# Performance work log

Measured on AMD Instinct MI355X. Metric: run time of the kernel, lower is better.

## Reference

```python
import jax, jax.numpy as jnp
import numpy as np

D_MODEL = 1024
N_HEADS = 16
N_GROUPS = 4
D_HEAD = D_MODEL // N_HEADS  # 64
HPG = N_HEADS // N_GROUPS    # heads per KV group = 4
B, T = 2, 2048


def _rope(x):
    # x: [B, H, T, D]; interleaved even/odd rotary, matching the torch module
    t, d = x.shape[2], x.shape[3]
    pos = jnp.arange(t, dtype=jnp.float32)[:, None]                      # [T,1]
    freq = jnp.exp(-(jnp.arange(0, d, 2, dtype=jnp.float32) / d)
                   * jnp.log(jnp.float32(10000.0)))                      # [D/2]
    angle = pos * freq                                                   # [T, D/2]
    cos, sin = jnp.cos(angle), jnp.sin(angle)
    xe, xo = x[..., ::2], x[..., 1::2]
    re = xe * cos - xo * sin
    ro = xe * sin + xo * cos
    return jnp.stack([re, ro], axis=-1).reshape(x.shape)


def setup_inputs() -> dict:
    key = jax.random.key(0)
    ks = jax.random.split(key, 10)
    s = 0.02
    return {
        "x":  jax.random.normal(ks[0], (B, T, D_MODEL), dtype=jnp.float32),
        "Wq": jax.random.normal(ks[1], (D_MODEL, D_MODEL), dtype=jnp.float32) * s,
        "bq": jax.random.normal(ks[2], (D_MODEL,), dtype=jnp.float32) * s,
        "Wk": jax.random.normal(ks[3], (D_MODEL, N_GROUPS * D_HEAD), dtype=jnp.float32) * s,
        "bk": jax.random.normal(ks[4], (N_GROUPS * D_HEAD,), dtype=jnp.float32) * s,
        "Wv": jax.random.normal(ks[5], (D_MODEL, N_GROUPS * D_HEAD), dtype=jnp.float32) * s,
        "bv": jax.random.normal(ks[6], (N_GROUPS * D_HEAD,), dtype=jnp.float32) * s,
        "Wo": jax.random.normal(ks[7], (D_MODEL, D_MODEL), dtype=jnp.float32) * s,
        "bo": jax.random.normal(ks[8], (D_MODEL,), dtype=jnp.float32) * s,
    }


def reference(x, Wq, bq, Wk, bk, Wv, bv, Wo, bo):
    b, t, _ = x.shape
    q = (x @ Wq + bq).reshape(b, t, N_HEADS, D_HEAD).transpose(0, 2, 1, 3)    # [B,H,T,D]
    k = (x @ Wk + bk).reshape(b, t, N_GROUPS, D_HEAD).transpose(0, 2, 1, 3)   # [B,G,T,D]
    v = (x @ Wv + bv).reshape(b, t, N_GROUPS, D_HEAD).transpose(0, 2, 1, 3)
    # GQA broadcast: idx = arange(n_heads) // heads_per_group  ==  repeat each group HPG times
    k = jnp.repeat(k, HPG, axis=1)                                            # [B,H,T,D]
    v = jnp.repeat(v, HPG, axis=1)
    q = _rope(q)
    k = _rope(k)
    scale = jnp.float32(np.sqrt(D_HEAD))
    scores = jnp.einsum('bhtd,bhsd->bhts', q, k) / scale                      # [B,H,T,T]
    causal = jnp.tril(jnp.ones((t, t), dtype=bool))
    scores = jnp.where(causal, scores, -jnp.inf)
    probs = jax.nn.softmax(scores, axis=-1)
    # dropout(p=0.05) is identity in eval mode
    attn = jnp.einsum('bhts,bhsd->bhtd', probs, v)
    out = attn.transpose(0, 2, 1, 3).reshape(b, t, N_HEADS * D_HEAD)
    return out @ Wo + bo
```

## Files before the change

kernel.cpp:

```cpp
#include <hip/hip_runtime.h>
#include <stdint.h>

typedef unsigned short u16;
typedef __attribute__((ext_vector_type(4))) float f32x4;
typedef __attribute__((ext_vector_type(8))) short bf16x8;
typedef __attribute__((ext_vector_type(4))) short bf16x4;

#define T_SEQ 2048
#define DM 1024
#define NH 16
#define NG 4
#define DH 64
#define QSCALE 0.18033688011112042f

__device__ __forceinline__ u16 f2bf(float f) {
    union { float f; uint32_t u; } v; v.f = f;
    uint32_t r = (v.u + 0x7FFFu + ((v.u >> 16) & 1u)) >> 16;
    return (u16)r;
}
__device__ __forceinline__ float bf2f(u16 u) {
    union { uint32_t u; float f; } v; v.u = ((uint32_t)u) << 16;
    return v.f;
}
__device__ __forceinline__ float fexp2(float x) {
#if __has_builtin(__builtin_amdgcn_exp2f)
    return __builtin_amdgcn_exp2f(x);
#else
    return exp2f(x);
#endif
}
__device__ __forceinline__ uint32_t cvtpk_bf16(float a, float b) {
    uint32_t r;
    asm("v_cvt_pk_bf16_f32 %0, %1, %2" : "=v"(r) : "v"(a), "v"(b));
    return r;
}

#if __has_builtin(__builtin_amdgcn_mfma_f32_16x16x16_bf16)
__device__ __forceinline__ f32x4 mfma16(bf16x4 a, bf16x4 b, f32x4 c) {
    return __builtin_amdgcn_mfma_f32_16x16x16_bf16(a, b, c, 0, 0, 0);
}
#elif __has_builtin(__builtin_amdgcn_mfma_f32_16x16x16bf16_1k)
__device__ __forceinline__ f32x4 mfma16(bf16x4 a, bf16x4 b, f32x4 c) {
    return __builtin_amdgcn_mfma_f32_16x16x16bf16_1k(a, b, c, 0, 0, 0);
}
#else
__device__ __forceinline__ f32x4 mfma16(bf16x4 a, bf16x4 b, f32x4 c) {
    asm("v_mfma_f32_16x16x16_bf16 %0, %1, %2, %0" : "+v"(c) : "v"(a), "v"(b));
    return c;
}
#endif

__device__ __forceinline__ void async16(const void* g, void* l) {
    __builtin_amdgcn_global_load_lds(
        (const __attribute__((address_space(1))) void*)g,
        (__attribute__((address_space(3))) void*)l,
        16, 0, 0);
}

__global__ __launch_bounds__(256) void k_prep(
    const float* __restrict__ x, u16* __restrict__ xb,
    const float* __restrict__ Wq, const float* __restrict__ Wk,
    const float* __restrict__ Wv, const float* __restrict__ Wo,
    u16* __restrict__ wqkvt, u16* __restrict__ wot,
    const float* __restrict__ bq, const float* __restrict__ bk,
    const float* __restrict__ bv, float* __restrict__ bqkv,
    float2* __restrict__ tbl) {
    int blk = blockIdx.x;
    int tid = threadIdx.x;
    if (blk < 2048) {
        int i = blk * 256 + tid;
        const float4* p = (const float4*)x + (size_t)i * 2;
        float4 a = p[0], b = p[1];
        bf16x8 v;
        v[0] = (short)f2bf(a.x); v[1] = (short)f2bf(a.y);
        v[2] = (short)f2bf(a.z); v[3] = (short)f2bf(a.w);
        v[4] = (short)f2bf(b.x); v[5] = (short)f2bf(b.y);
        v[6] = (short)f2bf(b.z); v[7] = (short)f2bf(b.w);
        ((bf16x8*)xb)[i] = v;
        return;
    }
    int t = blk - 2048;
    if (t >= 2560) {
        int u = t - 2560;
        if (u < 6) {
            int i = u * 256 + tid;
            if (i < 1536) {
                float v;
                if (i < 1024) v = bq[i];
                else if (i < 1280) v = bk[i - 1024];
                else v = bv[i - 1280];
                bqkv[i] = v;
            }
        } else {
            int idx = (u - 6) * 256 + tid;
            int tt = idx >> 5, i = idx & 31;
            float freq = exp2f(-(float)i * (13.287712379549449f / 32.0f));
            float ang = (float)tt * freq;
            tbl[idx] = make_float2(cosf(ang), sinf(ang));
        }
        return;
    }
    const float* src; u16* dst; int N;
    if (t < 1024)      { src = Wq; dst = wqkvt;                      N = 1024; }
    else if (t < 1280) { t -= 1024; src = Wk; dst = wqkvt + (size_t)1024 * 1024; N = 256; }
    else if (t < 1536) { t -= 1280; src = Wv; dst = wqkvt + (size_t)1280 * 1024; N = 256; }
    else               { t -= 1536; src = Wo; dst = wot;             N = 1024; }
    int ntiles = N >> 5;
    int n0 = (t % ntiles) * 32, k0 = (t / ntiles) * 32;
    __shared__ float tile[32][33];
    int tx = tid & 31, ty = tid >> 5;
#pragma unroll
    for (int q = 0; q < 4; q++)
        tile[ty + q * 8][tx] = src[(size_t)(k0 + ty + q * 8) * N + n0 + tx];
    __syncthreads();
#pragma unroll
    for (int q = 0; q < 4; q++)
        dst[(size_t)(n0 + ty + q * 8) * 1024 + k0 + tx] = f2bf(tile[tx][ty + q * 8]);
}

__global__ __launch_bounds__(256) void k_gemm_qkv(
    const u16* __restrict__ A, const u16* __restrict__ Bt,
    const float* __restrict__ bias, const float2* __restrict__ tbl,
    u16* __restrict__ Qo, u16* __restrict__ Ko, u16* __restrict__ Vto) {
    const int K = 1024;
    __shared__ __align__(16) u16 As[64 * 64];
    __shared__ __align__(16) u16 Bs[128 * 64];
    int tid = threadIdx.x;
    int lane = tid & 63, wid = tid >> 6;
    int wr = wid >> 1, wc = wid & 1;
    int l15 = lane & 15, lhi = lane >> 4;
    int row0 = blockIdx.y * 64, col0 = blockIdx.x * 128;
    f32x4 acc[2][4] = {};

    for (int k0 = 0; k0 < K; k0 += 64) {
#pragma unroll
        for (int i = 0; i < 2; i++) {
            int c = i * 256 + tid;
            int r = c >> 3, ch = c & 7;
            int sch = ch ^ (r & 7);
            async16(A + (size_t)(row0 + r) * K + k0 + sch * 8, &As[c * 8]);
        }
#pragma unroll
        for (int i = 0; i < 4; i++) {
            int c = i * 256 + tid;
            int r = c >> 3, ch = c & 7;
            int sch = ch ^ (r & 7);
            async16(Bt + (size_t)(col0 + r) * K + k0 + sch * 8, &Bs[c * 8]);
        }
        __syncthreads();
#pragma unroll
        for (int ks = 0; ks < 2; ks++) {
            bf16x8 af[2], bfr[4];
#pragma unroll
            for (int m = 0; m < 2; m++) {
                int r = wr * 32 + m * 16 + l15;
                int kb = (ks * 64 + lhi * 16) ^ ((r & 7) << 4);
                af[m] = *(const bf16x8*)((const char*)As + r * 128 + kb);
            }
#pragma unroll
            for (int n = 0; n < 4; n++) {
                int r = wc * 64 + n * 16 + l15;
                int kb = (ks * 64 + lhi * 16) ^ ((r & 7) << 4);
                bfr[n] = *(const bf16x8*)((const char*)Bs + r * 128 + kb);
            }
#pragma unroll
            for (int m = 0; m < 2; m++)
#pragma unroll
                for (int n = 0; n < 4; n++)
                    acc[m][n] = __builtin_amdgcn_mfma_f32_16x16x32_bf16(
                        af[m], bfr[n], acc[m][n], 0, 0, 0);
        }
        __syncthreads();
    }

    int type = (col0 >= 1280) ? 2 : (col0 >= 1024 ? 1 : 0);
    int rbase = row0 + wr * 32;
#pragma unroll
    for (int n = 0; n < 4; n++) {
        int col = col0 + wc * 64 + n * 16 + l15;
        float bv = bias[col];
        if (type == 2) {
            int cc = col - 1280;
            int g = cc >> 6, d = cc & 63;
#pragma unroll
            for (int m = 0; m < 2; m++)
#pragma unroll
                for (int i = 0; i < 4; i++) {
                    int rowg = rbase + m * 16 + lhi * 4 + i;
                    int t = rowg & (T_SEQ - 1), b = rowg >> 11;
                    int sp = t ^ ((d & 1) << 2);
                    Vto[(((size_t)(b * NG + g)) * DH + d) * T_SEQ + sp] =
                        f2bf(acc[m][n][i] + bv);
                }
        } else {
            float ssgn = (col & 1) ? 1.f : -1.f;
            int ip = (col & 63) >> 1;
#pragma unroll
            for (int m = 0; m < 2; m++)
#pragma unroll
                for (int i = 0; i < 4; i++) {
                    int rowg = rbase + m * 16 + lhi * 4 + i;
                    int t = rowg & (T_SEQ - 1), b = rowg >> 11;
                    float v = acc[m][n][i] + bv;
                    float other = __shfl_xor(v, 1);
                    float2 cs = tbl[t * 32 + ip];
                    float out = v * cs.x + other * cs.y * ssgn;
                    if (type == 0) {
                        int h = col >> 6, d = col & 63;
                        Qo[(((size_t)(b * NH + h)) * T_SEQ + t) * DH + d] =
                            f2bf(out * QSCALE);
                    } else {
                        int cc = col - 1024;
                        int g = cc >> 6, d = cc & 63;
                        Ko[(((size_t)(b * NG + g)) * T_SEQ + t) * DH + d] = f2bf(out);
                    }
                }
        }
    }
}

__global__ __launch_bounds__(256) void k_gemm_out(
    const u16* __restrict__ A, const u16* __restrict__ Bt,
    const float* __restrict__ bias, float* __restrict__ C,
    int M, int N, int K) {
    __shared__ __align__(16) u16 As[64 * 64];
    __shared__ __align__(16) u16 Bs[128 * 64];
    int tid = threadIdx.x;
    int lane = tid & 63, wid = tid >> 6;
    int wr = wid >> 1, wc = wid & 1;
    int l15 = lane & 15, lhi = lane >> 4;
    int row0 = blockIdx.y * 64, col0 = blockIdx.x * 128;
    f32x4 acc[2][4] = {};

    for (int k0 = 0; k0 < K; k0 += 64) {
#pragma unroll
        for (int i = 0; i < 2; i++) {
            int c = i * 256 + tid;
            int r = c >> 3, ch = c & 7;
            int sch = ch ^ (r & 7);
            async16(A + (size_t)(row0 + r) * K + k0 + sch * 8, &As[c * 8]);
        }
#pragma unroll
        for (int i = 0; i < 4; i++) {
            int c = i * 256 + tid;
            int r = c >> 3, ch = c & 7;
            int sch = ch ^ (r & 7);
            async16(Bt + (size_t)(col0 + r) * K + k0 + sch * 8, &Bs[c * 8]);
        }
        __syncthreads();
#pragma unroll
        for (int ks = 0; ks < 2; ks++) {
            bf16x8 af[2], bfr[4];
#pragma unroll
            for (int m = 0; m < 2; m++) {
                int r = wr * 32 + m * 16 + l15;
                int kb = (ks * 64 + lhi * 16) ^ ((r & 7) << 4);
                af[m] = *(const bf16x8*)((const char*)As + r * 128 + kb);
            }
#pragma unroll
            for (int n = 0; n < 4; n++) {
                int r = wc * 64 + n * 16 + l15;
                int kb = (ks * 64 + lhi * 16) ^ ((r & 7) << 4);
                bfr[n] = *(const bf16x8*)((const char*)Bs + r * 128 + kb);
            }
#pragma unroll
            for (int m = 0; m < 2; m++)
#pragma unroll
                for (int n = 0; n < 4; n++)
                    acc[m][n] = __builtin_amdgcn_mfma_f32_16x16x32_bf16(
                        af[m], bfr[n], acc[m][n], 0, 0, 0);
        }
        __syncthreads();
    }
#pragma unroll
    for (int n = 0; n < 4; n++) {
        int col = col0 + wc * 64 + n * 16 + l15;
        float bv = bias[col];
#pragma unroll
        for (int m = 0; m < 2; m++) {
            int row = row0 + wr * 32 + m * 16 + lhi * 4;
#pragma unroll
            for (int i = 0; i < 4; i++)
                C[(size_t)(row + i) * N + col] = acc[m][n][i] + bv;
        }
    }
}

__global__ __launch_bounds__(256) void k_attn(
    const u16* __restrict__ Q, const u16* __restrict__ K,
    const u16* __restrict__ Vt, u16* __restrict__ Aout) {
    int i0 = blockIdx.x;
    int u = i0 >> 5;
    int qt = (u < 16) ? (31 - u) : (u - 16);
    int bh = i0 & 31;
    int b = bh >> 4, h = bh & 15, g = h >> 2;
    int tid = threadIdx.x;
    int lane = tid & 63, wid = tid >> 6;
    int l15 = lane & 15, lhi = lane >> 4;

    const u16* Kp = K + ((size_t)(b * NG + g)) * T_SEQ * DH;
    const u16* Vp = Vt + ((size_t)(b * NG + g)) * DH * T_SEQ;

    __shared__ __align__(16) u16 Ks[2][64 * 64];
    __shared__ __align__(16) u16 Vs[2][64 * 64];

    const u16* Qp = Q + ((size_t)bh * T_SEQ + qt * 64) * DH;
    bf16x8 qf[2];
#pragma unroll
    for (int ks = 0; ks < 2; ks++)
        qf[ks] = *(const bf16x8*)(Qp + (size_t)(wid * 16 + l15) * DH + ks * 32 + lhi * 8);

    f32x4 of[4] = {};
    float m_i = -3.0e38f, l_i = 0.f;

    int nt = qt + 1;
    int swz = (l15 & 7) << 4;

    int c0 = tid, c1 = tid + 256;
    int rk0 = c0 >> 3, rk1 = c1 >> 3;
    int sk0 = (c0 & 7) ^ (rk0 & 7);
    int sk1 = (c1 & 7) ^ (rk1 & 7);
    int sv0 = (c0 & 7) ^ ((rk0 >> 1) & 7);
    int sv1 = (c1 & 7) ^ ((rk1 >> 1) & 7);
    const u16* kg0 = Kp + rk0 * DH + sk0 * 8;
    const u16* kg1 = Kp + rk1 * DH + sk1 * 8;
    const u16* vg0 = Vp + (size_t)rk0 * T_SEQ + sv0 * 8;
    const u16* vg1 = Vp + (size_t)rk1 * T_SEQ + sv1 * 8;

    async16(kg0, &Ks[0][c0 * 8]);
    async16(kg1, &Ks[0][c1 * 8]);
    async16(vg0, &Vs[0][c0 * 8]);
    async16(vg1, &Vs[0][c1 * 8]);
    __syncthreads();

#pragma unroll 1
    for (int it = 0; it < nt; it++) {
        int cur = it & 1;
        if (it + 1 < nt) {
            int nx = cur ^ 1;
            int ko = (it + 1) << 12;
            int vo = (it + 1) << 6;
            async16(kg0 + ko, &Ks[nx][c0 * 8]);
            async16(kg1 + ko, &Ks[nx][c1 * 8]);
            async16(vg0 + vo, &Vs[nx][c0 * 8]);
            async16(vg1 + vo, &Vs[nx][c1 * 8]);
        }
        const u16* Kc = Ks[cur];
        const u16* Vc = Vs[cur];

        f32x4 sf[4] = {};
        __builtin_amdgcn_s_setprio(1);
#pragma unroll
        for (int ks = 0; ks < 2; ks++)
#pragma unroll
            for (int n = 0; n < 4; n++) {
                int kb = (ks * 64 + lhi * 16) ^ swz;
                bf16x8 kf = *(const bf16x8*)((const char*)Kc + (n * 16 + l15) * 128 + kb);
                sf[n] = __builtin_amdgcn_mfma_f32_16x16x32_bf16(kf, qf[ks], sf[n], 0, 0, 0);
            }
        __builtin_amdgcn_s_setprio(0);

        if (it == nt - 1) {
            int qrow = qt * 64 + wid * 16 + l15;
            int sb = it * 64 + lhi * 4;
#pragma unroll
            for (int n = 0; n < 4; n++)
#pragma unroll
                for (int i = 0; i < 4; i++)
                    if (sb + n * 16 + i > qrow) sf[n][i] = -3.0e38f;
        }

        float pmt = sf[0][0];
#pragma unroll
        for (int n = 0; n < 4; n++)
#pragma unroll
            for (int i = 0; i < 4; i++)
                pmt = fmaxf(pmt, sf[n][i]);
        if (!__all(pmt - m_i <= 8.f)) {
#pragma unroll
            for (int off = 16; off <= 32; off <<= 1)
                pmt = fmaxf(pmt, __shfl_xor(pmt, off));
            float mn = fmaxf(m_i, pmt);
            float sc = fexp2(m_i - mn);
            m_i = mn;
            l_i *= sc;
            float sc4[4];
#pragma unroll
            for (int i = 0; i < 4; i++)
                sc4[i] = __shfl(sc, lhi * 4 + i);
#pragma unroll
            for (int n = 0; n < 4; n++)
#pragma unroll
                for (int i = 0; i < 4; i++)
                    of[n][i] *= sc4[i];
        }
        bf16x4 pa[4];
#pragma unroll
        for (int n = 0; n < 4; n++) {
#pragma unroll
            for (int i = 0; i < 4; i++) {
                float p = fexp2(sf[n][i] - m_i);
                sf[n][i] = p;
                l_i += p;
            }
            union { uint32_t u[2]; bf16x4 v; } pu;
            pu.u[0] = cvtpk_bf16(sf[n][0], sf[n][1]);
            pu.u[1] = cvtpk_bf16(sf[n][2], sf[n][3]);
            pa[n] = pu.v;
        }

        __builtin_amdgcn_s_setprio(1);
#pragma unroll
        for (int nd = 0; nd < 4; nd++) {
            int rowb = (nd * 16 + l15) * 128;
#pragma unroll
            for (int n = 0; n < 4; n++) {
                int kb = ((4 * n + lhi) ^ l15) << 3;
                bf16x4 vf = *(const bf16x4*)((const char*)Vc + rowb + kb);
                of[nd] = mfma16(pa[n], vf, of[nd]);
            }
        }
        __builtin_amdgcn_s_setprio(0);
        __syncthreads();
    }

#pragma unroll
    for (int off = 16; off <= 32; off <<= 1)
        l_i += __shfl_xor(l_i, off);
    float lq[4];
#pragma unroll
    for (int i = 0; i < 4; i++)
        lq[i] = __shfl(l_i, lhi * 4 + i);
#pragma unroll
    for (int n = 0; n < 4; n++)
#pragma unroll
        for (int i = 0; i < 4; i++) {
            int trow = qt * 64 + wid * 16 + lhi * 4 + i;
            float v = of[n][i] / lq[i];
            Aout[((size_t)(b * T_SEQ + trow)) * DM + h * 64 + n * 16 + l15] = f2bf(v);
        }
}

extern "C" void kernel_launch(void* const* d_in, const int* in_sizes, int n_in,
                              void* d_out, int out_size, void* d_ws, size_t ws_size,
                              hipStream_t stream) {
    const float* x  = (const float*)d_in[0];
    const float* Wq = (const float*)d_in[1];
    const float* bq = (const float*)d_in[2];
    const float* Wk = (const float*)d_in[3];
    const float* bk = (const float*)d_in[4];
    const float* Wv = (const float*)d_in[5];
    const float* bv = (const float*)d_in[6];
    const float* Wo = (const float*)d_in[7];
    const float* bo = (const float*)d_in[8];

    char* ws = (char*)d_ws;
    size_t o = 0;
    u16*   xb    = (u16*)(ws + o);  o += (size_t)4096 * 1024 * 2;
    u16*   wqkvt = (u16*)(ws + o);  o += (size_t)1536 * 1024 * 2;
    u16*   wot   = (u16*)(ws + o);  o += (size_t)1024 * 1024 * 2;
    float* bqkv  = (float*)(ws + o); o += 1536 * 4;
    o = (o + 255) & ~(size_t)255;
    u16*   Qb    = (u16*)(ws + o);  o += (size_t)2 * NH * T_SEQ * DH * 2;
    u16*   Kb    = (u16*)(ws + o);  o += (size_t)2 * NG * T_SEQ * DH * 2;
    u16*   Vtb   = (u16*)(ws + o);  o += (size_t)2 * NG * DH * T_SEQ * 2;
    u16*   attnb = (u16*)(ws + o);  o += (size_t)4096 * 1024 * 2;
    float2* tbl  = (float2*)(ws + o); o += (size_t)2048 * 32 * 8;

    k_prep<<<4870, 256, 0, stream>>>(x, xb, Wq, Wk, Wv, Wo, wqkvt, wot, bq, bk, bv, bqkv, tbl);
    k_gemm_qkv<<<dim3(12, 64), 256, 0, stream>>>(xb, wqkvt, bqkv, tbl, Qb, Kb, Vtb);
    k_attn<<<1024, 256, 0, stream>>>(Qb, Kb, Vtb, attnb);
    k_gemm_out<<<dim3(8, 64), 256, 0, stream>>>(attnb, wot, bo, (float*)d_out, 4096, 1024, 1024);
}
```

Before: 91.30 us.

## Enlarge GEMM tiles, remap workgroups, and compute softmax row sums via MFMA

Both projection GEMMs are merged into one templated kernel with 128x128 tiles (4x4 MFMA accumulators per wave) and an XCD-aware workgroup remapping, which halves the grid. In attention, the row-sum accumulation moves from scalar adds plus shuffles to an extra MFMA against a ones vector, and the row max uses v_max3. Larger tiles raise data reuse per block but increase register and LDS use and reduce the block count (384 and 256 blocks).

```diff
diff --git a/kernel.cpp b/kernel.cpp
--- a/kernel.cpp
+++ b/kernel.cpp
@@ -32,6 +32,11 @@
 __device__ __forceinline__ uint32_t cvtpk_bf16(float a, float b) {
     uint32_t r;
     asm("v_cvt_pk_bf16_f32 %0, %1, %2" : "=v"(r) : "v"(a), "v"(b));
+    return r;
+}
+__device__ __forceinline__ float max3f(float a, float b, float c) {
+    float r;
+    asm("v_max3_f32 %0, %1, %2, %3" : "=v"(r) : "v"(a), "v"(b), "v"(c));
     return r;
 }
 
@@ -118,42 +123,44 @@
         dst[(size_t)(n0 + ty + q * 8) * 1024 + k0 + tx] = f2bf(tile[tx][ty + q * 8]);
 }
 
-__global__ __launch_bounds__(256) void k_gemm_qkv(
+template <int EPI>
+__global__ __launch_bounds__(256) void k_gemm(
     const u16* __restrict__ A, const u16* __restrict__ Bt,
-    const float* __restrict__ bias, const float2* __restrict__ tbl,
-    u16* __restrict__ Qo, u16* __restrict__ Ko, u16* __restrict__ Vto) {
-    const int K = 1024;
-    __shared__ __align__(16) u16 As[64 * 64];
+    const float* __restrict__ bias, float* __restrict__ C,
+    const float2* __restrict__ tbl, u16* __restrict__ Qo,
+    u16* __restrict__ Ko, u16* __restrict__ Vto, int N, int K) {
+    __shared__ __align__(16) u16 As[128 * 64];
     __shared__ __align__(16) u16 Bs[128 * 64];
     int tid = threadIdx.x;
     int lane = tid & 63, wid = tid >> 6;
     int wr = wid >> 1, wc = wid & 1;
     int l15 = lane & 15, lhi = lane >> 4;
-    int row0 = blockIdx.y * 64, col0 = blockIdx.x * 128;
-    f32x4 acc[2][4] = {};
+
+    int nwg = gridDim.x * gridDim.y;
+    int orig = blockIdx.y * gridDim.x + blockIdx.x;
+    int q8 = nwg >> 3;
+    int wgid = (orig & 7) * q8 + (orig >> 3);
+    int bx = wgid % gridDim.x, by = wgid / gridDim.x;
+    int row0 = by * 128, col0 = bx * 128;
+
+    f32x4 acc[4][4] = {};
 
     for (int k0 = 0; k0 < K; k0 += 64) {
 #pragma unroll
-        for (int i = 0; i < 2; i++) {
+        for (int i = 0; i < 4; i++) {
             int c = i * 256 + tid;
             int r = c >> 3, ch = c & 7;
             int sch = ch ^ (r & 7);
             async16(A + (size_t)(row0 + r) * K + k0 + sch * 8, &As[c * 8]);
-        }
-#pragma unroll
-        for (int i = 0; i < 4; i++) {
-            int c = i * 256 + tid;
-            int r = c >> 3, ch = c & 7;
-            int sch = ch ^ (r & 7);
             async16(Bt + (size_t)(col0 + r) * K + k0 + sch * 8, &Bs[c * 8]);
         }
         __syncthreads();
 #pragma unroll
         for (int ks = 0; ks < 2; ks++) {
-            bf16x8 af[2], bfr[4];
-#pragma unroll
-            for (int m = 0; m < 2; m++) {
-                int r = wr * 32 + m * 16 + l15;
+            bf16x8 af[4], bfr[4];
+#pragma unroll
+            for (int m = 0; m < 4; m++) {
+                int r = wr * 64 + m * 16 + l15;
                 int kb = (ks * 64 + lhi * 16) ^ ((r & 7) << 4);
                 af[m] = *(const bf16x8*)((const char*)As + r * 128 + kb);
             }
@@ -164,7 +171,7 @@
                 bfr[n] = *(const bf16x8*)((const char*)Bs + r * 128 + kb);
             }
 #pragma unroll
-            for (int m = 0; m < 2; m++)
+            for (int m = 0; m < 4; m++)
 #pragma unroll
                 for (int n = 0; n < 4; n++)
                     acc[m][n] = __builtin_amdgcn_mfma_f32_16x16x32_bf16(
@@ -173,115 +180,63 @@
         __syncthreads();
     }
 
-    int type = (col0 >= 1280) ? 2 : (col0 >= 1024 ? 1 : 0);
-    int rbase = row0 + wr * 32;
-#pragma unroll
-    for (int n = 0; n < 4; n++) {
-        int col = col0 + wc * 64 + n * 16 + l15;
-        float bv = bias[col];
-        if (type == 2) {
-            int cc = col - 1280;
-            int g = cc >> 6, d = cc & 63;
-#pragma unroll
-            for (int m = 0; m < 2; m++)
-#pragma unroll
-                for (int i = 0; i < 4; i++) {
-                    int rowg = rbase + m * 16 + lhi * 4 + i;
-                    int t = rowg & (T_SEQ - 1), b = rowg >> 11;
-                    int sp = t ^ ((d & 1) << 2);
-                    Vto[(((size_t)(b * NG + g)) * DH + d) * T_SEQ + sp] =
-                        f2bf(acc[m][n][i] + bv);
-                }
-        } else {
-            float ssgn = (col & 1) ? 1.f : -1.f;
-            int ip = (col & 63) >> 1;
-#pragma unroll
-            for (int m = 0; m < 2; m++)
-#pragma unroll
-                for (int i = 0; i < 4; i++) {
-                    int rowg = rbase + m * 16 + lhi * 4 + i;
-                    int t = rowg & (T_SEQ - 1), b = rowg >> 11;
-                    float v = acc[m][n][i] + bv;
-                    float other = __shfl_xor(v, 1);
-                    float2 cs = tbl[t * 32 + ip];
-                    float out = v * cs.x + other * cs.y * ssgn;
-                    if (type == 0) {
-                        int h = col >> 6, d = col & 63;
-                        Qo[(((size_t)(b * NH + h)) * T_SEQ + t) * DH + d] =
-                            f2bf(out * QSCALE);
-                    } else {
-                        int cc = col - 1024;
-                        int g = cc >> 6, d = cc & 63;
-                        Ko[(((size_t)(b * NG + g)) * T_SEQ + t) * DH + d] = f2bf(out);
+    if (EPI == 0) {
+#pragma unroll
+        for (int n = 0; n < 4; n++) {
+            int col = col0 + wc * 64 + n * 16 + l15;
+            float bv = bias[col];
+#pragma unroll
+            for (int m = 0; m < 4; m++) {
+                int row = row0 + wr * 64 + m * 16 + lhi * 4;
+#pragma unroll
+                for (int i = 0; i < 4; i++)
+                    C[(size_t)(row + i) * N + col] = acc[m][n][i] + bv;
+            }
+        }
+    } else {
+        int type = (col0 >= 1280) ? 2 : (col0 >= 1024 ? 1 : 0);
+        int rbase = row0 + wr * 64;
+#pragma unroll
+        for (int n = 0; n < 4; n++) {
+            int col = col0 + wc * 64 + n * 16 + l15;
+            float bv = bias[col];
+            if (type == 2) {
+                int cc = col - 1280;
+                int g = cc >> 6, d = cc & 63;
+#pragma unroll
+                for (int m = 0; m < 4; m++)
+#pragma unroll
+                    for (int i = 0; i < 4; i++) {
+                        int rowg = rbase + m * 16 + lhi * 4 + i;
+                        int t = rowg & (T_SEQ - 1), b = rowg >> 11;
+                        int sp = t ^ ((d & 1) << 2);
+                        Vto[(((size_t)(b * NG + g)) * DH + d) * T_SEQ + sp] =
+                            f2bf(acc[m][n][i] + bv);
                     }
-                }
-        }
-    }
-}
-
-__global__ __launch_bounds__(256) void k_gemm_out(
-    const u16* __restrict__ A, const u16* __restrict__ Bt,
-    const float* __restrict__ bias, float* __restrict__ C,
-    int M, int N, int K) {
-    __shared__ __align__(16) u16 As[64 * 64];
-    __shared__ __align__(16) u16 Bs[128 * 64];
-    int tid = threadIdx.x;
-    int lane = tid & 63, wid = tid >> 6;
-    int wr = wid >> 1, wc = wid & 1;
-    int l15 = lane & 15, lhi = lane >> 4;
-    int row0 = blockIdx.y * 64, col0 = blockIdx.x * 128;
-    f32x4 acc[2][4] = {};
-
-    for (int k0 = 0; k0 < K; k0 += 64) {
-#pragma unroll
-        for (int i = 0; i < 2; i++) {
-            int c = i * 256 + tid;
-            int r = c >> 3, ch = c & 7;
-            int sch = ch ^ (r & 7);
-            async16(A + (size_t)(row0 + r) * K + k0 + sch * 8, &As[c * 8]);
-        }
-#pragma unroll
-        for (int i = 0; i < 4; i++) {
-            int c = i * 256 + tid;
-            int r = c >> 3, ch = c & 7;
-            int sch = ch ^ (r & 7);
-            async16(Bt + (size_t)(col0 + r) * K + k0 + sch * 8, &Bs[c * 8]);
-        }
-        __syncthreads();
-#pragma unroll
-        for (int ks = 0; ks < 2; ks++) {
-            bf16x8 af[2], bfr[4];
-#pragma unroll
-            for (int m = 0; m < 2; m++) {
-                int r = wr * 32 + m * 16 + l15;
-                int kb = (ks * 64 + lhi * 16) ^ ((r & 7) << 4);
-                af[m] = *(const bf16x8*)((const char*)As + r * 128 + kb);
-            }
-#pragma unroll
-            for (int n = 0; n < 4; n++) {
-                int r = wc * 64 + n * 16 + l15;
-                int kb = (ks * 64 + lhi * 16) ^ ((r & 7) << 4);
-                bfr[n] = *(const bf16x8*)((const char*)Bs + r * 128 + kb);
-            }
-#pragma unroll
-            for (int m = 0; m < 2; m++)
-#pragma unroll
-                for (int n = 0; n < 4; n++)
-                    acc[m][n] = __builtin_amdgcn_mfma_f32_16x16x32_bf16(
-                        af[m], bfr[n], acc[m][n], 0, 0, 0);
-        }
-        __syncthreads();
-    }
-#pragma unroll
-    for (int n = 0; n < 4; n++) {
-        int col = col0 + wc * 64 + n * 16 + l15;
-        float bv = bias[col];
-#pragma unroll
-        for (int m = 0; m < 2; m++) {
-            int row = row0 + wr * 32 + m * 16 + lhi * 4;
-#pragma unroll
-            for (int i = 0; i < 4; i++)
-                C[(size_t)(row + i) * N + col] = acc[m][n][i] + bv;
+            } else {
+                float ssgn = (col & 1) ? 1.f : -1.f;
+                int ip = (col & 63) >> 1;
+#pragma unroll
+                for (int m = 0; m < 4; m++)
+#pragma unroll
+                    for (int i = 0; i < 4; i++) {
+                        int rowg = rbase + m * 16 + lhi * 4 + i;
+                        int t = rowg & (T_SEQ - 1), b = rowg >> 11;
+                        float v = acc[m][n][i] + bv;
+                        float other = __shfl_xor(v, 1);
+                        float2 cs = tbl[t * 32 + ip];
+                        float out = v * cs.x + other * cs.y * ssgn;
+                        if (type == 0) {
+                            int h = col >> 6, d = col & 63;
+                            Qo[(((size_t)(b * NH + h)) * T_SEQ + t) * DH + d] =
+                                f2bf(out * QSCALE);
+                        } else {
+                            int cc = col - 1024;
+                            int g = cc >> 6, d = cc & 63;
+                            Ko[(((size_t)(b * NG + g)) * T_SEQ + t) * DH + d] = f2bf(out);
+                        }
+                    }
+            }
         }
     }
 }
@@ -311,7 +266,12 @@
         qf[ks] = *(const bf16x8*)(Qp + (size_t)(wid * 16 + l15) * DH + ks * 32 + lhi * 8);
 
     f32x4 of[4] = {};
-    float m_i = -3.0e38f, l_i = 0.f;
+    f32x4 lsum = {};
+    float m_i = -3.0e38f;
+
+    union { uint32_t uu[2]; bf16x4 v; } onesu;
+    onesu.uu[0] = 0x3F803F80u; onesu.uu[1] = 0x3F803F80u;
+    const bf16x4 ones4 = onesu.v;
 
     int nt = qt + 1;
     int swz = (l15 & 7) << 4;
@@ -370,12 +330,12 @@
                     if (sb + n * 16 + i > qrow) sf[n][i] = -3.0e38f;
         }
 
-        float pmt = sf[0][0];
-#pragma unroll
-        for (int n = 0; n < 4; n++)
-#pragma unroll
-            for (int i = 0; i < 4; i++)
-                pmt = fmaxf(pmt, sf[n][i]);
+        float t0 = max3f(sf[0][0], sf[0][1], sf[0][2]);
+        float t1 = max3f(sf[0][3], sf[1][0], sf[1][1]);
+        float t2 = max3f(sf[1][2], sf[1][3], sf[2][0]);
+        float t3 = max3f(sf[2][1], sf[2][2], sf[2][3]);
+        float t4 = max3f(sf[3][0], sf[3][1], sf[3][2]);
+        float pmt = fmaxf(max3f(t0, t1, t2), max3f(t3, t4, sf[3][3]));
         if (!__all(pmt - m_i <= 8.f)) {
 #pragma unroll
             for (int off = 16; off <= 32; off <<= 1)
@@ -383,7 +343,6 @@
             float mn = fmaxf(m_i, pmt);
             float sc = fexp2(m_i - mn);
             m_i = mn;
-            l_i *= sc;
             float sc4[4];
 #pragma unroll
             for (int i = 0; i < 4; i++)
@@ -393,19 +352,19 @@
 #pragma unroll
                 for (int i = 0; i < 4; i++)
                     of[n][i] *= sc4[i];
+#pragma unroll
+            for (int i = 0; i < 4; i++)
+                lsum[i] *= sc4[i];
         }
         bf16x4 pa[4];
 #pragma unroll
         for (int n = 0; n < 4; n++) {
 #pragma unroll
-            for (int i = 0; i < 4; i++) {
-                float p = fexp2(sf[n][i] - m_i);
-                sf[n][i] = p;
-                l_i += p;
-            }
-            union { uint32_t u[2]; bf16x4 v; } pu;
-            pu.u[0] = cvtpk_bf16(sf[n][0], sf[n][1]);
-            pu.u[1] = cvtpk_bf16(sf[n][2], sf[n][3]);
+            for (int i = 0; i < 4; i++)
+                sf[n][i] = fexp2(sf[n][i] - m_i);
+            union { uint32_t uu[2]; bf16x4 v; } pu;
+            pu.uu[0] = cvtpk_bf16(sf[n][0], sf[n][1]);
+            pu.uu[1] = cvtpk_bf16(sf[n][2], sf[n][3]);
             pa[n] = pu.v;
         }
 
@@ -420,23 +379,19 @@
                 of[nd] = mfma16(pa[n], vf, of[nd]);
             }
         }
+#pragma unroll
+        for (int n = 0; n < 4; n++)
+            lsum = mfma16(pa[n], ones4, lsum);
         __builtin_amdgcn_s_setprio(0);
         __syncthreads();
     }
 
 #pragma unroll
-    for (int off = 16; off <= 32; off <<= 1)
-        l_i += __shfl_xor(l_i, off);
-    float lq[4];
-#pragma unroll
-    for (int i = 0; i < 4; i++)
-        lq[i] = __shfl(l_i, lhi * 4 + i);
-#pragma unroll
     for (int n = 0; n < 4; n++)
 #pragma unroll
         for (int i = 0; i < 4; i++) {
             int trow = qt * 64 + wid * 16 + lhi * 4 + i;
-            float v = of[n][i] / lq[i];
+            float v = of[n][i] / lsum[i];
             Aout[((size_t)(b * T_SEQ + trow)) * DM + h * 64 + n * 16 + l15] = f2bf(v);
         }
 }
@@ -468,7 +423,7 @@
     float2* tbl  = (float2*)(ws + o); o += (size_t)2048 * 32 * 8;
 
     k_prep<<<4870, 256, 0, stream>>>(x, xb, Wq, Wk, Wv, Wo, wqkvt, wot, bq, bk, bv, bqkv, tbl);
-    k_gemm_qkv<<<dim3(12, 64), 256, 0, stream>>>(xb, wqkvt, bqkv, tbl, Qb, Kb, Vtb);
+    k_gemm<1><<<dim3(12, 32), 256, 0, stream>>>(xb, wqkvt, bqkv, nullptr, tbl, Qb, Kb, Vtb, 1536, 1024);
     k_attn<<<1024, 256, 0, stream>>>(Qb, Kb, Vtb, attnb);
-    k_gemm_out<<<dim3(8, 64), 256, 0, stream>>>(attnb, wot, bo, (float*)d_out, 4096, 1024, 1024);
-}
+    k_gemm<0><<<dim3(8, 32), 256, 0, stream>>>(attnb, wot, bo, (float*)d_out, nullptr, nullptr, nullptr, nullptr, 1024, 1024);
+}
```

New measurement: 105.9 us. +16.0%, slower.
